# Kernel tuning notes

Measured on AMD Instinct MI355X. Metric: run time of the kernel, lower is better.

## Reference

```python
import jax, jax.numpy as jnp
import numpy as np

B, T, D_IN = 2, 2048, 1024
H, D_HEAD = 16, 64
D_INNER = H * D_HEAD  # 1024
D_OUT = D_HEAD        # out_proj maps d_inner -> d_out


def setup_inputs() -> dict:
    key = jax.random.key(0)
    ks = jax.random.split(key, 6)
    s_in = 1.0 / np.sqrt(D_IN)
    s_inner = 1.0 / np.sqrt(D_INNER)
    return {
        "x": jax.random.normal(ks[0], (B, T, D_IN), dtype=jnp.float32),
        "Wq": jax.random.uniform(ks[1], (D_IN, D_INNER), jnp.float32, -s_in, s_in),
        "Wk": jax.random.uniform(ks[2], (D_IN, D_INNER), jnp.float32, -s_in, s_in),
        "Wv": jax.random.uniform(ks[3], (D_IN, D_INNER), jnp.float32, -s_in, s_in),
        "Wo": jax.random.uniform(ks[4], (D_INNER, D_OUT), jnp.float32, -s_inner, s_inner),
        "bo": jax.random.uniform(ks[5], (D_OUT,), jnp.float32, -s_inner, s_inner),
    }


def reference(x, Wq, Wk, Wv, Wo, bo):
    b, t, _ = x.shape
    # projections -> [b, h, t, d]
    def split_heads(y):
        return y.reshape(b, t, H, D_HEAD).transpose(0, 2, 1, 3)
    q = split_heads(x @ Wq)
    k = split_heads(x @ Wk)
    v = split_heads(x @ Wv)
    scores = jnp.einsum("bhqd,bhkd->bhqk", q, k)
    causal = jnp.triu(jnp.ones((t, t), dtype=bool), k=1)
    scores = jnp.where(causal, -jnp.inf, scores)
    # NOTE: original scales by sqrt(d_out*num_heads), not sqrt(head_dim)
    attn = jax.nn.softmax(scores / np.sqrt(D_INNER), axis=-1)
    y = jnp.einsum("bhqk,bhkd->bhqd", attn, v)
    y = y.transpose(0, 2, 1, 3).reshape(b, t, D_INNER)
    return y @ Wo + bo
```

## Files before the change

kernel.cpp:

```cpp
#include <hip/hip_runtime.h>
#include <hip/hip_bf16.h>

typedef __attribute__((ext_vector_type(8))) short short8;
typedef __attribute__((ext_vector_type(4))) float f32x4;
typedef __attribute__((ext_vector_type(8))) unsigned short ushort8v;


__device__ __forceinline__ unsigned short f2bf(float f) {
  union { float f; unsigned int u; } x; x.f = f;
  unsigned int r = x.u + 0x7FFFu + ((x.u >> 16) & 1u);
  return (unsigned short)(r >> 16);
}

__device__ __forceinline__ unsigned int pk2bf(float lo, float hi) {
  __hip_bfloat162 b2 = __float22bfloat162_rn(make_float2(lo, hi));
  union { __hip_bfloat162 b; unsigned int u; } c; c.b = b2;
  return c.u;
}

__device__ __forceinline__ void gload_lds16(const void* g, void* l) {
  __builtin_amdgcn_global_load_lds(
      (const __attribute__((address_space(1))) void*)g,
      (__attribute__((address_space(3))) void*)l, 16, 0, 0);
}


__global__ __launch_bounds__(256) void prep(
    const float* __restrict__ x,
    const float* __restrict__ Wq, const float* __restrict__ Wk, const float* __restrict__ Wv,
    const float* __restrict__ Wo, const float* __restrict__ bo,
    unsigned short* __restrict__ xb,
    unsigned short* __restrict__ wqt, unsigned short* __restrict__ wkt,
    unsigned short* __restrict__ wvt, unsigned short* __restrict__ wot,
    float* __restrict__ out) {
  __shared__ float tile[32][33];
  int b = blockIdx.x;
  if (b < 4096) {
    int i = (b * 256 + threadIdx.x) * 4;
    float4 f = *(const float4*)(x + i);
    ushort4 o;
    o.x = f2bf(f.x); o.y = f2bf(f.y); o.z = f2bf(f.z); o.w = f2bf(f.w);
    *(ushort4*)(xb + i) = o;
  } else if (b < 7168) {
    int idx = b - 4096;
    int z = idx >> 10, rem = idx & 1023;
    const float* src = (z == 0) ? Wq : (z == 1) ? Wk : Wv;
    unsigned short* dst = (z == 0) ? wqt : (z == 1) ? wkt : wvt;
    int kx = (rem & 31) * 32, ny = (rem >> 5) * 32;
    int tx = threadIdx.x & 31, ty = threadIdx.x >> 5;
    #pragma unroll
    for (int r = 0; r < 32; r += 8)
      tile[ty + r][tx] = src[(size_t)(kx + ty + r) * 1024 + ny + tx];
    __syncthreads();
    #pragma unroll
    for (int r = 0; r < 32; r += 8)
      dst[(size_t)(ny + ty + r) * 1024 + kx + tx] = f2bf(tile[tx][ty + r]);
  } else if (b < 7232) {
    int idx = b - 7168;
    int kx = (idx & 31) * 32, ny = (idx >> 5) * 32;
    int tx = threadIdx.x & 31, ty = threadIdx.x >> 5;
    #pragma unroll
    for (int r = 0; r < 32; r += 8)
      tile[ty + r][tx] = Wo[(size_t)(kx + ty + r) * 64 + ny + tx];
    __syncthreads();
    #pragma unroll
    for (int r = 0; r < 32; r += 8)
      wot[(size_t)(ny + ty + r) * 1024 + kx + tx] = f2bf(tile[tx][ty + r]);
  } else {
    int t = (b - 7232) * 256 + threadIdx.x;
    float4 bi = *(const float4*)(bo + (t & 15) * 4);
    *(float4*)(out + (size_t)t * 4) = bi;
  }
}


__global__ __launch_bounds__(512, 2) void qkv_gemm2(
    const unsigned short* __restrict__ Xb,
    const unsigned short* __restrict__ Wstk,
    unsigned short* __restrict__ Oq, unsigned short* __restrict__ Ok,
    unsigned short* __restrict__ Ovt) {
  constexpr int Kd = 1024, BK = 32, NT = Kd / BK;
  __shared__ __align__(16) unsigned short As[3][256 * 32];
  __shared__ __align__(16) unsigned short Bs[3][256 * 32];

  int wg = blockIdx.x;
  int swz8 = (wg & 7) * 24 + (wg >> 3);
  int mt = swz8 >> 4, ntile = swz8 & 15;
  int m0 = mt * 256, n0 = ntile * 256;

  int tid = threadIdx.x, lane = tid & 63, wave = tid >> 6;
  int wm = wave >> 2, wn = wave & 3;
  int l15 = lane & 15, quad = lane >> 4;

  int srow0 = tid >> 2, sg0 = tid & 3;
  int srow1 = (tid + 512) >> 2, sg1 = (tid + 512) & 3;
  int ga0 = (sg0 ^ (srow0 & 3)) * 8, ga1 = (sg1 ^ (srow1 & 3)) * 8;

  f32x4 acc[8][4] = {};

  {
    gload_lds16(Wstk + (size_t)(m0 + srow0) * Kd + 0 + ga0, &As[0][tid * 8]);
    gload_lds16(Wstk + (size_t)(m0 + srow1) * Kd + 0 + ga1, &As[0][(tid + 512) * 8]);
    gload_lds16(Xb + (size_t)(n0 + srow0) * Kd + 0 + ga0, &Bs[0][tid * 8]);
    gload_lds16(Xb + (size_t)(n0 + srow1) * Kd + 0 + ga1, &Bs[0][(tid + 512) * 8]);
    gload_lds16(Wstk + (size_t)(m0 + srow0) * Kd + BK + ga0, &As[1][tid * 8]);
    gload_lds16(Wstk + (size_t)(m0 + srow1) * Kd + BK + ga1, &As[1][(tid + 512) * 8]);
    gload_lds16(Xb + (size_t)(n0 + srow0) * Kd + BK + ga0, &Bs[1][tid * 8]);
    gload_lds16(Xb + (size_t)(n0 + srow1) * Kd + BK + ga1, &Bs[1][(tid + 512) * 8]);
  }

  int cur = 0;
  for (int i = 0; i < NT; ++i) {
    if (i < NT - 1) { asm volatile("s_waitcnt vmcnt(4)" ::: "memory"); }
    else            { asm volatile("s_waitcnt vmcnt(0)" ::: "memory"); }
    __builtin_amdgcn_s_barrier();
    __builtin_amdgcn_sched_barrier(0);

    if (i + 2 < NT) {
      int s2 = cur + 2; if (s2 >= 3) s2 -= 3;
      int k0 = (i + 2) * BK;
      gload_lds16(Wstk + (size_t)(m0 + srow0) * Kd + k0 + ga0, &As[s2][tid * 8]);
      gload_lds16(Wstk + (size_t)(m0 + srow1) * Kd + k0 + ga1, &As[s2][(tid + 512) * 8]);
      gload_lds16(Xb + (size_t)(n0 + srow0) * Kd + k0 + ga0, &Bs[s2][tid * 8]);
      gload_lds16(Xb + (size_t)(n0 + srow1) * Kd + k0 + ga1, &Bs[s2][(tid + 512) * 8]);
    }

    {
      const unsigned short* Ab = As[cur];
      const unsigned short* Bb = Bs[cur];
      short8 bfr[4];
      #pragma unroll
      for (int ni = 0; ni < 4; ++ni) {
        int row = wn * 64 + ni * 16 + l15;
        bfr[ni] = *(const short8*)&Bb[row * 32 + ((quad ^ (row & 3)) * 8)];
      }
      __builtin_amdgcn_s_setprio(1);
      #pragma unroll
      for (int mi = 0; mi < 8; ++mi) {
        int row = wm * 128 + mi * 16 + l15;
        short8 af = *(const short8*)&Ab[row * 32 + ((quad ^ (row & 3)) * 8)];
        #pragma unroll
        for (int ni = 0; ni < 4; ++ni)
          acc[mi][ni] = __builtin_amdgcn_mfma_f32_16x16x32_bf16(af, bfr[ni], acc[mi][ni], 0, 0, 0);
      }
      __builtin_amdgcn_s_setprio(0);
    }
    if (++cur == 3) cur = 0;
  }

  int region = mt >> 2;
  if (region < 2) {
    unsigned short* O = (region == 0) ? Oq : Ok;
    float scale = (region == 0) ? 0.0450842200f : 1.0f;
    #pragma unroll
    for (int mi = 0; mi < 8; ++mi) {
      int dg = (m0 - region * 1024) + wm * 128 + mi * 16 + quad * 4;
      int h = dg >> 6, d0 = dg & 63;
      #pragma unroll
      for (int ni = 0; ni < 4; ++ni) {
        int t = n0 + wn * 64 + ni * 16 + l15;
        int b = t >> 11, tt = t & 2047;
        uint2 pk;
        pk.x = pk2bf(acc[mi][ni][0] * scale, acc[mi][ni][1] * scale);
        pk.y = pk2bf(acc[mi][ni][2] * scale, acc[mi][ni][3] * scale);
        *(uint2*)(O + (((size_t)(b * 16 + h) * 2048 + tt) << 6) + d0) = pk;
      }
    }
  } else {
    #pragma unroll
    for (int mi = 0; mi < 8; ++mi) {
      int dg = (m0 - 2048) + wm * 128 + mi * 16 + quad * 4;
      int h = dg >> 6, d0 = dg & 63;
      #pragma unroll
      for (int ni = 0; ni < 4; ++ni) {
        int t = n0 + wn * 64 + ni * 16 + l15;
        int b = t >> 11, tt = t & 2047;
        #pragma unroll
        for (int r = 0; r < 4; ++r)
          Ovt[(((size_t)(b * 16 + h) * 64 + d0 + r) << 11) + tt] = f2bf(acc[mi][ni][r]);
      }
    }
  }
}


__global__ __launch_bounds__(256, 4) void attn13(
    const unsigned short* __restrict__ Qg, const unsigned short* __restrict__ Kg,
    const unsigned short* __restrict__ Vtg, const unsigned short* __restrict__ Wot,
    float* __restrict__ out) {
  constexpr int T = 2048;
  __shared__ __align__(16) unsigned short Ks[2][64 * 64];
  __shared__ __align__(16) unsigned short Vs[2][64 * 64];
  __shared__ __align__(16) unsigned short Ps[4][16 * 64];
  int bh = blockIdx.x;
  int by = blockIdx.y;
  int g = by >> 3, w8 = by & 7;
  int qt = (g == 0) ? w8 : (g == 1) ? (15 - w8) : (g == 2) ? (16 + w8) : (31 - w8);
  int tid = threadIdx.x, lane = tid & 63, wave = tid >> 6;
  int l15 = lane & 15, quad = lane >> 4;
  int swz = l15 & 7;
  const unsigned short* Qb = Qg + (size_t)bh * T * 64;
  const unsigned short* Kb = Kg + (size_t)bh * T * 64;
  const unsigned short* Vb = Vtg + (size_t)bh * 64 * T;
  int h = bh & 15, b = bh >> 4;
  int qw = qt * 64 + wave * 16;

  short8 qf[2];
  #pragma unroll
  for (int s = 0; s < 2; ++s)
    qf[s] = *(const short8*)(Qb + (size_t)(qw + l15) * 64 + quad * 8 + 32 * s);

  f32x4 Oacc[4] = {};
  float m_run = -__builtin_inff();
  float l_run = 0.f;

  int srow = tid >> 3, sc8 = tid & 7;
  int sdst = srow * 64 + ((sc8 ^ (srow & 7)) * 8);

  ushort8v kpre[2], vpre[2];
  #pragma unroll
  for (int r = 0; r < 2; ++r) {
    kpre[r] = *(const ushort8v*)(Kb + (size_t)(srow + 32 * r) * 64 + sc8 * 8);
    vpre[r] = *(const ushort8v*)(Vb + (size_t)(srow + 32 * r) * T + sc8 * 8);
  }
  *(ushort8v*)&Ks[0][sdst] = kpre[0];
  *(ushort8v*)&Ks[0][sdst + 2048] = kpre[1];
  *(ushort8v*)&Vs[0][sdst] = vpre[0];
  *(ushort8v*)&Vs[0][sdst + 2048] = vpre[1];
  __syncthreads();

  for (int kt = 0; kt <= qt; ++kt) {
    const unsigned short* Kl = Ks[kt & 1];
    const unsigned short* Vl = Vs[kt & 1];
    unsigned short* Kn = Ks[(kt & 1) ^ 1];
    unsigned short* Vn = Vs[(kt & 1) ^ 1];

    if (kt < qt) {
      #pragma unroll
      for (int r = 0; r < 2; ++r) {
        kpre[r] = *(const ushort8v*)(Kb + (size_t)((kt + 1) * 64 + srow + 32 * r) * 64 + sc8 * 8);
        vpre[r] = *(const ushort8v*)(Vb + (size_t)(srow + 32 * r) * T + (kt + 1) * 64 + sc8 * 8);
      }
    }

    f32x4 S[4] = {};
    __builtin_amdgcn_s_setprio(1);
    #pragma unroll
    for (int s = 0; s < 2; ++s)
      #pragma unroll
      for (int mi = 0; mi < 4; ++mi) {
        short8 kf = *(const short8*)&Kl[(mi * 16 + l15) * 64 + ((quad + 4 * s) ^ swz) * 8];
        S[mi] = __builtin_amdgcn_mfma_f32_16x16x32_bf16(kf, qf[s], S[mi], 0, 0, 0);
      }
    __builtin_amdgcn_s_setprio(0);

    if (kt == qt) {
      int ql = wave * 16 + l15;
      #pragma unroll
      for (int mi = 0; mi < 4; ++mi) {
        int tokl = mi * 16 + quad * 4;
        #pragma unroll
        for (int r = 0; r < 4; ++r)
          if (tokl + r > ql) S[mi][r] = -__builtin_inff();
      }
    }

    float t0 = fmaxf(fmaxf(S[0][0], S[0][1]), fmaxf(S[0][2], S[0][3]));
    float t1 = fmaxf(fmaxf(S[1][0], S[1][1]), fmaxf(S[1][2], S[1][3]));
    float t2 = fmaxf(fmaxf(S[2][0], S[2][1]), fmaxf(S[2][2], S[2][3]));
    float t3 = fmaxf(fmaxf(S[3][0], S[3][1]), fmaxf(S[3][2], S[3][3]));
    float vmax = fmaxf(fmaxf(t0, t1), fmaxf(t2, t3));
    vmax = fmaxf(vmax, __shfl_xor(vmax, 16));
    vmax = fmaxf(vmax, __shfl_xor(vmax, 32));
    float mold = m_run;
    bool defer = __all(vmax - mold <= 8.f) != 0;
    float mnew = defer ? mold : fmaxf(mold, vmax);
    float alpha = defer ? 1.f : __builtin_amdgcn_exp2f(mold - mnew);
    m_run = mnew;
    float rs = 0.f;
    #pragma unroll
    for (int mi = 0; mi < 4; ++mi) {
      float p0 = __builtin_amdgcn_exp2f(S[mi][0] - mnew);
      float p1 = __builtin_amdgcn_exp2f(S[mi][1] - mnew);
      float p2 = __builtin_amdgcn_exp2f(S[mi][2] - mnew);
      float p3 = __builtin_amdgcn_exp2f(S[mi][3] - mnew);
      rs += (p0 + p1) + (p2 + p3);
      uint2 pk;
      pk.x = pk2bf(p0, p1);
      pk.y = pk2bf(p2, p3);
      int gg = (2 * mi + (quad >> 1)) ^ swz;
      *(uint2*)&Ps[wave][l15 * 64 + gg * 8 + (quad & 1) * 4] = pk;
    }
    rs += __shfl_xor(rs, 16);
    rs += __shfl_xor(rs, 32);
    l_run = l_run * alpha + rs;

    if (!defer)
      #pragma unroll
      for (int jd = 0; jd < 4; ++jd)
        #pragma unroll
        for (int r = 0; r < 4; ++r)
          Oacc[jd][r] *= alpha;

    if (kt < qt) {
      *(ushort8v*)&Kn[sdst] = kpre[0];
      *(ushort8v*)&Kn[sdst + 2048] = kpre[1];
      *(ushort8v*)&Vn[sdst] = vpre[0];
      *(ushort8v*)&Vn[sdst + 2048] = vpre[1];
    }

    __builtin_amdgcn_s_setprio(1);
    #pragma unroll
    for (int s = 0; s < 2; ++s) {
      short8 pf = *(const short8*)&Ps[wave][l15 * 64 + ((quad + 4 * s) ^ swz) * 8];
      #pragma unroll
      for (int jd = 0; jd < 4; ++jd) {
        short8 vfr = *(const short8*)&Vl[(jd * 16 + l15) * 64 + ((quad + 4 * s) ^ swz) * 8];
        Oacc[jd] = __builtin_amdgcn_mfma_f32_16x16x32_bf16(vfr, pf, Oacc[jd], 0, 0, 0);
      }
    }
    __builtin_amdgcn_s_setprio(0);
    if (kt < qt) __syncthreads();
  }

  {
    float linv = 1.f / l_run;
    unsigned short* Yl = &Ps[wave][0];
    #pragma unroll
    for (int jd = 0; jd < 4; ++jd) {
      uint2 pk;
      pk.x = pk2bf(Oacc[jd][0] * linv, Oacc[jd][1] * linv);
      pk.y = pk2bf(Oacc[jd][2] * linv, Oacc[jd][3] * linv);
      int gg = (jd * 2 + (quad >> 1)) ^ swz;
      *(uint2*)&Yl[l15 * 64 + gg * 8 + (quad & 1) * 4] = pk;
    }
    short8 wof[4][2];
    #pragma unroll
    for (int nt = 0; nt < 4; ++nt)
      #pragma unroll
      for (int s = 0; s < 2; ++s)
        wof[nt][s] = *(const short8*)(Wot + (size_t)(nt * 16 + l15) * 1024 + h * 64 + quad * 8 + 32 * s);
    f32x4 acc2[4] = {};
    #pragma unroll
    for (int s = 0; s < 2; ++s) {
      short8 ya = *(const short8*)&Yl[l15 * 64 + (((quad + 4 * s) ^ swz) * 8)];
      #pragma unroll
      for (int nt = 0; nt < 4; ++nt)
        acc2[nt] = __builtin_amdgcn_mfma_f32_16x16x32_bf16(ya, wof[nt][s], acc2[nt], 0, 0, 0);
    }
    int q0 = b * 2048 + qt * 64 + wave * 16 + quad * 4;
    #pragma unroll
    for (int nt = 0; nt < 4; ++nt)
      #pragma unroll
      for (int r = 0; r < 4; ++r)
        atomicAdd(&out[(size_t)(q0 + r) * 64 + nt * 16 + l15], acc2[nt][r]);
  }
}


extern "C" void kernel_launch(void* const* d_in, const int* in_sizes, int n_in,
                              void* d_out, int out_size, void* d_ws, size_t ws_size,
                              hipStream_t stream) {
  const float* x  = (const float*)d_in[0];
  const float* Wq = (const float*)d_in[1];
  const float* Wk = (const float*)d_in[2];
  const float* Wv = (const float*)d_in[3];
  const float* Wo = (const float*)d_in[4];
  const float* bo = (const float*)d_in[5];
  float* out = (float*)d_out;
  char* ws = (char*)d_ws;

  unsigned short* xb  = (unsigned short*)(ws);
  unsigned short* wqt = (unsigned short*)(ws + (8ull << 20));
  unsigned short* wkt = (unsigned short*)(ws + (10ull << 20));
  unsigned short* wvt = (unsigned short*)(ws + (12ull << 20));
  unsigned short* wot = (unsigned short*)(ws + (14ull << 20));
  unsigned short* q   = (unsigned short*)(ws + (15ull << 20));
  unsigned short* k   = (unsigned short*)(ws + (23ull << 20));
  unsigned short* vt  = (unsigned short*)(ws + (31ull << 20));

  prep<<<7488, 256, 0, stream>>>(x, Wq, Wk, Wv, Wo, bo, xb, wqt, wkt, wvt, wot, out);
  qkv_gemm2<<<192, 512, 0, stream>>>(xb, wqt, q, k, vt);
  attn13<<<dim3(32, 32), 256, 0, stream>>>(q, k, vt, wot, out);
}
```

Baseline: 168.5 us.

## Shrink QKV GEMM tiles to 128x128 with 4 waves and double buffering

The QKV projection GEMM moves from 256x256 tiles with 8 waves and a 3-stage LDS ring to 128x128 tiles with 4 waves and 2-stage double buffering, launched as 768 blocks instead of 192. The aim is to fill the 256 CUs better, since 192 large tiles leave many CUs idle, and to cut per-block LDS and register use so more blocks fit per CU. The LDS swizzle changes to suit the new row pattern. In exchange, each tile has lower arithmetic intensity, so more global/L2 traffic, and the wait is now vmcnt(0) every step, which shortens the load prefetch depth.

```diff
diff --git a/kernel.cpp b/kernel.cpp
--- a/kernel.cpp
+++ b/kernel.cpp
@@ -74,55 +74,47 @@
 }
 
 
-__global__ __launch_bounds__(512, 2) void qkv_gemm2(
+__global__ __launch_bounds__(256, 4) void qkv_gemm3(
     const unsigned short* __restrict__ Xb,
     const unsigned short* __restrict__ Wstk,
     unsigned short* __restrict__ Oq, unsigned short* __restrict__ Ok,
     unsigned short* __restrict__ Ovt) {
   constexpr int Kd = 1024, BK = 32, NT = Kd / BK;
-  __shared__ __align__(16) unsigned short As[3][256 * 32];
-  __shared__ __align__(16) unsigned short Bs[3][256 * 32];
+  __shared__ __align__(16) unsigned short As[2][128 * 32];
+  __shared__ __align__(16) unsigned short Bs[2][128 * 32];
 
   int wg = blockIdx.x;
-  int swz8 = (wg & 7) * 24 + (wg >> 3);
-  int mt = swz8 >> 4, ntile = swz8 & 15;
-  int m0 = mt * 256, n0 = ntile * 256;
+  int swz8 = (wg & 7) * 96 + (wg >> 3);
+  int mt = swz8 >> 5, ntile = swz8 & 31;
+  int m0 = mt * 128, n0 = ntile * 128;
 
   int tid = threadIdx.x, lane = tid & 63, wave = tid >> 6;
-  int wm = wave >> 2, wn = wave & 3;
+  int wm = wave >> 1, wn = wave & 1;
   int l15 = lane & 15, quad = lane >> 4;
 
-  int srow0 = tid >> 2, sg0 = tid & 3;
-  int srow1 = (tid + 512) >> 2, sg1 = (tid + 512) & 3;
-  int ga0 = (sg0 ^ (srow0 & 3)) * 8, ga1 = (sg1 ^ (srow1 & 3)) * 8;
-
-  f32x4 acc[8][4] = {};
-
-  {
-    gload_lds16(Wstk + (size_t)(m0 + srow0) * Kd + 0 + ga0, &As[0][tid * 8]);
-    gload_lds16(Wstk + (size_t)(m0 + srow1) * Kd + 0 + ga1, &As[0][(tid + 512) * 8]);
-    gload_lds16(Xb + (size_t)(n0 + srow0) * Kd + 0 + ga0, &Bs[0][tid * 8]);
-    gload_lds16(Xb + (size_t)(n0 + srow1) * Kd + 0 + ga1, &Bs[0][(tid + 512) * 8]);
-    gload_lds16(Wstk + (size_t)(m0 + srow0) * Kd + BK + ga0, &As[1][tid * 8]);
-    gload_lds16(Wstk + (size_t)(m0 + srow1) * Kd + BK + ga1, &As[1][(tid + 512) * 8]);
-    gload_lds16(Xb + (size_t)(n0 + srow0) * Kd + BK + ga0, &Bs[1][tid * 8]);
-    gload_lds16(Xb + (size_t)(n0 + srow1) * Kd + BK + ga1, &Bs[1][(tid + 512) * 8]);
-  }
-
-  int cur = 0;
+  int sr0 = tid >> 2, sg0 = tid & 3;
+  int sr1 = (tid + 256) >> 2, sg1 = (tid + 256) & 3;
+  int ga0 = (sg0 ^ ((sr0 >> 1) & 3)) * 8, ga1 = (sg1 ^ ((sr1 >> 1) & 3)) * 8;
+
+  f32x4 acc[4][4] = {};
+
+  gload_lds16(Wstk + (size_t)(m0 + sr0) * Kd + ga0, &As[0][tid * 8]);
+  gload_lds16(Wstk + (size_t)(m0 + sr1) * Kd + ga1, &As[0][(tid + 256) * 8]);
+  gload_lds16(Xb + (size_t)(n0 + sr0) * Kd + ga0, &Bs[0][tid * 8]);
+  gload_lds16(Xb + (size_t)(n0 + sr1) * Kd + ga1, &Bs[0][(tid + 256) * 8]);
+
   for (int i = 0; i < NT; ++i) {
-    if (i < NT - 1) { asm volatile("s_waitcnt vmcnt(4)" ::: "memory"); }
-    else            { asm volatile("s_waitcnt vmcnt(0)" ::: "memory"); }
+    int cur = i & 1;
+    asm volatile("s_waitcnt vmcnt(0)" ::: "memory");
     __builtin_amdgcn_s_barrier();
     __builtin_amdgcn_sched_barrier(0);
 
-    if (i + 2 < NT) {
-      int s2 = cur + 2; if (s2 >= 3) s2 -= 3;
-      int k0 = (i + 2) * BK;
-      gload_lds16(Wstk + (size_t)(m0 + srow0) * Kd + k0 + ga0, &As[s2][tid * 8]);
-      gload_lds16(Wstk + (size_t)(m0 + srow1) * Kd + k0 + ga1, &As[s2][(tid + 512) * 8]);
-      gload_lds16(Xb + (size_t)(n0 + srow0) * Kd + k0 + ga0, &Bs[s2][tid * 8]);
-      gload_lds16(Xb + (size_t)(n0 + srow1) * Kd + k0 + ga1, &Bs[s2][(tid + 512) * 8]);
+    if (i + 1 < NT) {
+      int k0 = (i + 1) * BK;
+      gload_lds16(Wstk + (size_t)(m0 + sr0) * Kd + k0 + ga0, &As[cur ^ 1][tid * 8]);
+      gload_lds16(Wstk + (size_t)(m0 + sr1) * Kd + k0 + ga1, &As[cur ^ 1][(tid + 256) * 8]);
+      gload_lds16(Xb + (size_t)(n0 + sr0) * Kd + k0 + ga0, &Bs[cur ^ 1][tid * 8]);
+      gload_lds16(Xb + (size_t)(n0 + sr1) * Kd + k0 + ga1, &Bs[cur ^ 1][(tid + 256) * 8]);
     }
 
     {
@@ -132,29 +124,28 @@
       #pragma unroll
       for (int ni = 0; ni < 4; ++ni) {
         int row = wn * 64 + ni * 16 + l15;
-        bfr[ni] = *(const short8*)&Bb[row * 32 + ((quad ^ (row & 3)) * 8)];
+        bfr[ni] = *(const short8*)&Bb[row * 32 + ((quad ^ ((row >> 1) & 3)) * 8)];
       }
       __builtin_amdgcn_s_setprio(1);
       #pragma unroll
-      for (int mi = 0; mi < 8; ++mi) {
-        int row = wm * 128 + mi * 16 + l15;
-        short8 af = *(const short8*)&Ab[row * 32 + ((quad ^ (row & 3)) * 8)];
+      for (int mi = 0; mi < 4; ++mi) {
+        int row = wm * 64 + mi * 16 + l15;
+        short8 af = *(const short8*)&Ab[row * 32 + ((quad ^ ((row >> 1) & 3)) * 8)];
         #pragma unroll
         for (int ni = 0; ni < 4; ++ni)
           acc[mi][ni] = __builtin_amdgcn_mfma_f32_16x16x32_bf16(af, bfr[ni], acc[mi][ni], 0, 0, 0);
       }
       __builtin_amdgcn_s_setprio(0);
     }
-    if (++cur == 3) cur = 0;
-  }
-
-  int region = mt >> 2;
+  }
+
+  int region = mt >> 3;
   if (region < 2) {
     unsigned short* O = (region == 0) ? Oq : Ok;
     float scale = (region == 0) ? 0.0450842200f : 1.0f;
     #pragma unroll
-    for (int mi = 0; mi < 8; ++mi) {
-      int dg = (m0 - region * 1024) + wm * 128 + mi * 16 + quad * 4;
+    for (int mi = 0; mi < 4; ++mi) {
+      int dg = (m0 - region * 1024) + wm * 64 + mi * 16 + quad * 4;
       int h = dg >> 6, d0 = dg & 63;
       #pragma unroll
       for (int ni = 0; ni < 4; ++ni) {
@@ -168,8 +159,8 @@
     }
   } else {
     #pragma unroll
-    for (int mi = 0; mi < 8; ++mi) {
-      int dg = (m0 - 2048) + wm * 128 + mi * 16 + quad * 4;
+    for (int mi = 0; mi < 4; ++mi) {
+      int dg = (m0 - 2048) + wm * 64 + mi * 16 + quad * 4;
       int h = dg >> 6, d0 = dg & 63;
       #pragma unroll
       for (int ni = 0; ni < 4; ++ni) {
@@ -380,6 +371,6 @@
   unsigned short* vt  = (unsigned short*)(ws + (31ull << 20));
 
   prep<<<7488, 256, 0, stream>>>(x, Wq, Wk, Wv, Wo, bo, xb, wqt, wkt, wvt, wot, out);
-  qkv_gemm2<<<192, 512, 0, stream>>>(xb, wqt, q, k, vt);
+  qkv_gemm3<<<768, 256, 0, stream>>>(xb, wqt, q, k, vt);
   attn13<<<dim3(32, 32), 256, 0, stream>>>(q, k, vt, wot, out);
 }
```

Result: faster. 152.4 us (-9.6%).
